# Optimization experiments

Hardware: AMD Instinct MI355X
Metric: run time of the kernel (lower is better)

## Reference

```python
import jax, jax.numpy as jnp
import numpy as np

MODES = 2
N = 6000
KNN = 15
NODES = 512
LC = 3  # number of hidden layers
SCALE = 0.05


def _gen_coo(n, knn):
    # One (row, col) pair per CK_inputs entry: node i couples to 2*(knn+1)
    # neighbors i-knn .. i+knn+1, clipped to valid range. Duplicates at the
    # boundaries are summed on scatter (matches torch sparse coalesce()).
    offsets = np.arange(-knn, knn + 2)            # 2*(knn+1) offsets
    rows = np.repeat(np.arange(n), 2 * (knn + 1))
    cols = np.clip((np.arange(n)[:, None] + offsets[None, :]).reshape(-1), 0, n - 1)
    return rows.astype(np.int32), cols.astype(np.int32)


def setup_inputs() -> dict:
    key = jax.random.key(0)
    k0, k1, k2, k3 = jax.random.split(key, 4)
    CK_inputs = jax.random.normal(k0, (N, 2 * (KNN + 1), 3), dtype=jnp.float32)
    W_in = (jax.random.normal(k1, (3, NODES), dtype=jnp.float32) * SCALE)
    b_in = jnp.zeros((NODES,), dtype=jnp.float32)
    Wh = (jax.random.normal(k2, (LC, NODES, NODES), dtype=jnp.float32) * SCALE)
    bh = jnp.zeros((LC, NODES), dtype=jnp.float32)
    W_out = (jax.random.normal(k3, (NODES, MODES ** 2), dtype=jnp.float32) * SCALE)
    b_out = jnp.zeros((MODES ** 2,), dtype=jnp.float32)
    rows_np, cols_np = _gen_coo(N, KNN)
    return {
        "CK_inputs": CK_inputs,
        "W_in": W_in, "b_in": b_in,
        "Wh": Wh, "bh": bh,
        "W_out": W_out, "b_out": b_out,
        "rows": jnp.asarray(rows_np), "cols": jnp.asarray(cols_np),
    }


def reference(CK_inputs, W_in, b_in, Wh, bh, W_out, b_out, rows, cols):
    n = CK_inputs.shape[0]
    modes = int(np.sqrt(b_out.shape[0]))
    # MLP over all E = N*2*(Knn+1) couplings: [E,3] -> [E, modes^2]
    x = CK_inputs.reshape(-1, 3)
    h = jax.nn.relu(x @ W_in + b_in)
    for l in range(Wh.shape[0]):  # small fixed layer count
        h = jax.nn.relu(h @ Wh[l] + bh[l])
    vals = (h @ W_out + b_out).reshape(-1, modes, modes)  # [E, mi, mj]
    # Fused scatter-add: original builds modes^2 sparse COO tensors with
    # indices (r*modes+mi, c*modes+mj), sums, coalesces, densifies. That is
    # exactly dense[r, mi, c, mj] += vals[e, mi, mj].
    dense = jnp.zeros((n, modes, n, modes), dtype=CK_inputs.dtype)
    dense = dense.at[rows, :, cols, :].add(vals)
    return dense.reshape(n * modes, n * modes)
```

## Files before the change

kernel.cpp:

```cpp
#include <hip/hip_runtime.h>

#define NN     6000
#define KNN    15
#define EPB    32
#define HID    512
#define NLAYER 3
#define OUTDIM 12000
#define MB     96
#define NTH    512
#define NKT    16
#define NG     (NLAYER * NKT)

typedef _Float16 half8  __attribute__((ext_vector_type(8)));
typedef _Float16 half4v __attribute__((ext_vector_type(4)));
typedef float    floatx4 __attribute__((ext_vector_type(4)));

__global__ void prep_weights(const float* __restrict__ Wh, _Float16* __restrict__ Wt)
{
    const int blk = blockIdx.x;
    const int ln  = threadIdx.x;
    const int nt  = blk & 31;
    const int kt  = (blk >> 5) & 15;
    const int l   = blk >> 9;
    const int lc  = ln & 15, lg = ln >> 4;
    const float* src = Wh + (size_t)l * HID * HID
                          + (size_t)(kt * 32 + lg * 8) * HID + nt * 16 + lc;
    half8 v;
#pragma unroll
    for (int j = 0; j < 8; ++j) v[j] = (_Float16)src[(size_t)j * HID];
    *(half8*)(Wt + (size_t)blk * 512 + ln * 8) = v;
}

__global__ __launch_bounds__(NTH, 1)
void mlp_mfma_kernel(const float* __restrict__ CK,
                     const float* __restrict__ W_in,
                     const float* __restrict__ b_in,
                     const float* __restrict__ bh,
                     const float* __restrict__ W_out,
                     const float* __restrict__ b_out,
                     const _Float16* __restrict__ Wt,
                     float4* __restrict__ vals)
{
    extern __shared__ float4 smem4[];
    _Float16* Ah = (_Float16*)smem4;
    __shared__ float xs[MB * 3];

    const int t  = threadIdx.x;
    const int w  = t >> 6;
    const int ln = t & 63;
    const int lc = ln & 15;
    const int lg = ln >> 4;
    const int kbase = lg * 8;
    const int swzA  = (lc & 7) << 3;

    const half8* __restrict__ Wt8 = (const half8*)Wt + (size_t)(w * 4) * 64 + ln;

    half8 bA[4], bB[4];
#pragma unroll
    for (int nf = 0; nf < 4; ++nf) bA[nf] = Wt8[(size_t)0 * 2048 + nf * 64];
#pragma unroll
    for (int nf = 0; nf < 4; ++nf) bB[nf] = Wt8[(size_t)1 * 2048 + nf * 64];

    if (t < MB * 3) xs[t] = CK[(size_t)blockIdx.x * (MB * 3) + t];
    __syncthreads();

    {
        const int j0 = t;
        const float wi0 = W_in[j0], wi1 = W_in[HID + j0], wi2 = W_in[2 * HID + j0];
        const float bi  = b_in[j0];
#pragma unroll 8
        for (int r = 0; r < MB; ++r) {
            float a = fmaf(xs[r * 3 + 2], wi2,
                      fmaf(xs[r * 3 + 1], wi1,
                      fmaf(xs[r * 3 + 0], wi0, bi)));
            Ah[r * HID + (j0 ^ ((r & 7) << 3))] = (_Float16)fmaxf(a, 0.f);
        }
    }
    __syncthreads();

#define KSTEP(G, RCUR) do {                                                    \
        half8 a_[6];                                                           \
        const int kb_ = ((G) & 15) * 32 + kbase;                               \
        _Pragma("unroll")                                                      \
        for (int mf_ = 0; mf_ < 6; ++mf_)                                      \
            a_[mf_] = *(const half8*)&Ah[(mf_ * 16 + lc) * HID + (kb_ ^ swzA)];\
        __builtin_amdgcn_s_setprio(1);                                         \
        _Pragma("unroll")                                                      \
        for (int mf_ = 0; mf_ < 6; ++mf_)                                      \
            _Pragma("unroll")                                                  \
            for (int nf_ = 0; nf_ < 4; ++nf_)                                  \
                acc[mf_][nf_] = __builtin_amdgcn_mfma_f32_16x16x32_f16(        \
                    RCUR[nf_], a_[mf_], acc[mf_][nf_], 0, 0, 0);               \
        __builtin_amdgcn_s_setprio(0);                                         \
        if ((G) + 2 < NG) {                                                    \
            _Pragma("unroll")                                                  \
            for (int nf_ = 0; nf_ < 4; ++nf_)                                  \
                RCUR[nf_] = Wt8[(size_t)((G) + 2) * 2048 + nf_ * 64];          \
        }                                                                      \
    } while (0)

    for (int layer = 0; layer < NLAYER; ++layer) {
        const float* __restrict__ bias = bh + layer * HID;

        floatx4 acc[6][4];
#pragma unroll
        for (int nf = 0; nf < 4; ++nf) {
            const floatx4 bv = *(const floatx4*)&bias[w * 64 + nf * 16 + lg * 4];
#pragma unroll
            for (int mf = 0; mf < 6; ++mf) acc[mf][nf] = bv;
        }

#pragma unroll
        for (int kt2 = 0; kt2 < NKT; kt2 += 2) {
            const int g = layer * NKT + kt2;
            KSTEP(g,     bA);
            KSTEP(g + 1, bB);
        }

        __syncthreads();
#pragma unroll
        for (int mf = 0; mf < 6; ++mf) {
            const int r = mf * 16 + lc;
#pragma unroll
            for (int nf = 0; nf < 4; ++nf) {
                const int n0 = w * 64 + nf * 16 + lg * 4;
                half4v h4;
#pragma unroll
                for (int j = 0; j < 4; ++j)
                    h4[j] = (_Float16)fmaxf(acc[mf][nf][j], 0.f);
                *(half4v*)&Ah[r * HID + (n0 ^ swzA)] = h4;
            }
        }
        __syncthreads();
    }

    {
        const int s = t & 7;
        const float4 bo = *(const float4*)b_out;
#pragma unroll
        for (int pass = 0; pass < 2; ++pass) {
            const int rr = pass * 64 + (t >> 3);
            if (rr < MB) {
                const int swzr = (rr & 7) << 3;
                float p0 = 0.f, p1 = 0.f, p2 = 0.f, p3 = 0.f;
                for (int i = 0; i < HID / 8; ++i) {
                    const int k = s + i * 8;
                    const float hv = (float)Ah[rr * HID + (k ^ swzr)];
                    const floatx4 wv = *(const floatx4*)&W_out[k * 4];
                    p0 = fmaf(hv, wv[0], p0);
                    p1 = fmaf(hv, wv[1], p1);
                    p2 = fmaf(hv, wv[2], p2);
                    p3 = fmaf(hv, wv[3], p3);
                }
#pragma unroll
                for (int m = 1; m < 8; m <<= 1) {
                    p0 += __shfl_xor(p0, m, 64);
                    p1 += __shfl_xor(p1, m, 64);
                    p2 += __shfl_xor(p2, m, 64);
                    p3 += __shfl_xor(p3, m, 64);
                }
                if (s == 0)
                    vals[(size_t)blockIdx.x * MB + rr] =
                        make_float4(p0 + bo.x, p1 + bo.y, p2 + bo.z, p3 + bo.w);
            }
        }
    }
}

__global__ __launch_bounds__(256, 8)
void write_out(const float4* __restrict__ vals, float* __restrict__ out)
{
    const int n = blockIdx.x;
    const int t = threadIdx.x;
    __shared__ float4 v[EPB];
    __shared__ float  band[2][2 * EPB];

    if (t < EPB) v[t] = vals[(size_t)n * EPB + t];
    const int cmin  = (n - KNN < 0) ? 0 : n - KNN;
    const int cmax  = (n + KNN + 1 > NN - 1) ? NN - 1 : n + KNN + 1;
    const int width = cmax - cmin + 1;
    __syncthreads();

    if (t < width) {
        const int c = cmin + t;
        int e_lo, e_hi;
        if (c == 0)           { e_lo = 0;                  e_hi = KNN - n; }
        else if (c == NN - 1) { e_lo = (NN - 1) - n + KNN; e_hi = EPB - 1; }
        else                  { e_lo = e_hi = c - n + KNN; }
        float s0 = 0.f, s1 = 0.f, s2 = 0.f, s3 = 0.f;
        for (int e = e_lo; e <= e_hi; ++e) {
            const float4 pv = v[e];
            s0 += pv.x; s1 += pv.y; s2 += pv.z; s3 += pv.w;
        }
        band[0][2 * t] = s0; band[0][2 * t + 1] = s1;
        band[1][2 * t] = s2; band[1][2 * t + 1] = s3;
    }
    __syncthreads();

    const int j0 = 2 * cmin;
    const int w2 = 2 * width;
#pragma unroll
    for (int mi = 0; mi < 2; ++mi) {
        float* rowp = out + (size_t)(2 * n + mi) * OUTDIM;
        for (int q = t; q < OUTDIM / 4; q += 256) {
            const int j = 4 * q;
            floatx4 o;
            o[0] = ((unsigned)(j + 0 - j0) < (unsigned)w2) ? band[mi][j + 0 - j0] : 0.f;
            o[1] = ((unsigned)(j + 1 - j0) < (unsigned)w2) ? band[mi][j + 1 - j0] : 0.f;
            o[2] = ((unsigned)(j + 2 - j0) < (unsigned)w2) ? band[mi][j + 2 - j0] : 0.f;
            o[3] = ((unsigned)(j + 3 - j0) < (unsigned)w2) ? band[mi][j + 3 - j0] : 0.f;
            __builtin_nontemporal_store(o, (floatx4*)(rowp + j));
        }
    }
}

extern "C" void kernel_launch(void* const* d_in, const int* in_sizes, int n_in,
                              void* d_out, int out_size, void* d_ws, size_t ws_size,
                              hipStream_t stream) {
    const float* CK    = (const float*)d_in[0];
    const float* W_in  = (const float*)d_in[1];
    const float* b_in  = (const float*)d_in[2];
    const float* Wh    = (const float*)d_in[3];
    const float* bh    = (const float*)d_in[4];
    const float* W_out = (const float*)d_in[5];
    const float* b_out = (const float*)d_in[6];
    float* out = (float*)d_out;

    _Float16* Wt   = (_Float16*)d_ws;
    float4*   vals = (float4*)((char*)d_ws + (size_t)3 * HID * HID * sizeof(_Float16));

    (void)ws_size;
    hipFuncSetAttribute((const void*)mlp_mfma_kernel,
                        hipFuncAttributeMaxDynamicSharedMemorySize, 98304);

    prep_weights<<<NLAYER * 16 * 32, 64, 0, stream>>>(Wh, Wt);
    mlp_mfma_kernel<<<NN / 3, NTH, 98304, stream>>>(CK, W_in, b_in, bh, W_out, b_out, Wt, vals);
    write_out<<<NN, 256, 0, stream>>>(vals, out);
}
```

Measured before the change: 412.8 us.

## Store activations in MFMA fragment-ordered LDS layout instead of XOR swizzle

Activations in LDS are reorganized so each (k-tile, m-fragment) block of 16 rows x 32 k values is stored contiguously in the order each lane reads it for the MFMA A operand. The input layer, the inter-layer writeback and the output projection are all rewritten to produce and consume this layout. This turns A-fragment loads into linear 16-byte-per-lane reads without XOR address math and lets the output layer read half8 vectors. The input layer now computes 8 contiguous k values per lane, with more W_in global loads per thread, and the writeback stores may see different bank patterns.

Measured after the change: 535.6 us. +29.7%, slower.

```diff
diff --git a/kernel.cpp b/kernel.cpp
--- a/kernel.cpp
+++ b/kernel.cpp
@@ -50,8 +50,6 @@
     const int ln = t & 63;
     const int lc = ln & 15;
     const int lg = ln >> 4;
-    const int kbase = lg * 8;
-    const int swzA  = (lc & 7) << 3;
 
     const half8* __restrict__ Wt8 = (const half8*)Wt + (size_t)(w * 4) * 64 + ln;
 
@@ -65,25 +63,32 @@
     __syncthreads();
 
     {
-        const int j0 = t;
-        const float wi0 = W_in[j0], wi1 = W_in[HID + j0], wi2 = W_in[2 * HID + j0];
-        const float bi  = b_in[j0];
-#pragma unroll 8
-        for (int r = 0; r < MB; ++r) {
-            float a = fmaf(xs[r * 3 + 2], wi2,
-                      fmaf(xs[r * 3 + 1], wi1,
-                      fmaf(xs[r * 3 + 0], wi0, bi)));
-            Ah[r * HID + (j0 ^ ((r & 7) << 3))] = (_Float16)fmaxf(a, 0.f);
+#pragma unroll
+        for (int i = 0; i < 12; ++i) {
+            const int b  = w + i * 8;
+            const int kt = b / 6, mf = b - kt * 6;
+            const int r  = mf * 16 + lc;
+            const int k0 = kt * 32 + lg * 8;
+            const float x0 = xs[r * 3 + 0], x1 = xs[r * 3 + 1], x2 = xs[r * 3 + 2];
+            half8 h;
+#pragma unroll
+            for (int j = 0; j < 8; ++j) {
+                const int k = k0 + j;
+                float a = fmaf(x2, W_in[2 * HID + k],
+                          fmaf(x1, W_in[HID + k],
+                          fmaf(x0, W_in[k], b_in[k])));
+                h[j] = (_Float16)fmaxf(a, 0.f);
+            }
+            *(half8*)&Ah[b * 512 + ln * 8] = h;
         }
     }
     __syncthreads();
 
 #define KSTEP(G, RCUR) do {                                                    \
         half8 a_[6];                                                           \
-        const int kb_ = ((G) & 15) * 32 + kbase;                               \
         _Pragma("unroll")                                                      \
         for (int mf_ = 0; mf_ < 6; ++mf_)                                      \
-            a_[mf_] = *(const half8*)&Ah[(mf_ * 16 + lc) * HID + (kb_ ^ swzA)];\
+            a_[mf_] = *(const half8*)&Ah[((((G) & 15) * 6 + mf_) << 9) + ln * 8]; \
         __builtin_amdgcn_s_setprio(1);                                         \
         _Pragma("unroll")                                                      \
         for (int mf_ = 0; mf_ < 6; ++mf_)                                      \
@@ -120,15 +125,15 @@
         __syncthreads();
 #pragma unroll
         for (int mf = 0; mf < 6; ++mf) {
-            const int r = mf * 16 + lc;
 #pragma unroll
             for (int nf = 0; nf < 4; ++nf) {
-                const int n0 = w * 64 + nf * 16 + lg * 4;
                 half4v h4;
 #pragma unroll
                 for (int j = 0; j < 4; ++j)
                     h4[j] = (_Float16)fmaxf(acc[mf][nf][j], 0.f);
-                *(half4v*)&Ah[r * HID + (n0 ^ swzA)] = h4;
+                const int ktp  = w * 2 + (nf >> 1);
+                const int slot = lc + 16 * (2 * (nf & 1) + (lg >> 1));
+                *(half4v*)&Ah[((ktp * 6 + mf) << 9) + slot * 8 + (lg & 1) * 4] = h4;
             }
         }
         __syncthreads();
@@ -141,16 +146,23 @@
         for (int pass = 0; pass < 2; ++pass) {
             const int rr = pass * 64 + (t >> 3);
             if (rr < MB) {
-                const int swzr = (rr & 7) << 3;
+                const int mf = rr >> 4, rl = rr & 15;
                 float p0 = 0.f, p1 = 0.f, p2 = 0.f, p3 = 0.f;
-                for (int i = 0; i < HID / 8; ++i) {
-                    const int k = s + i * 8;
-                    const float hv = (float)Ah[rr * HID + (k ^ swzr)];
-                    const floatx4 wv = *(const floatx4*)&W_out[k * 4];
-                    p0 = fmaf(hv, wv[0], p0);
-                    p1 = fmaf(hv, wv[1], p1);
-                    p2 = fmaf(hv, wv[2], p2);
-                    p3 = fmaf(hv, wv[3], p3);
+#pragma unroll
+                for (int i = 0; i < 8; ++i) {
+                    const int kb2 = i * 8 + s;
+                    const half8 hv8 = *(const half8*)
+                        &Ah[(((kb2 >> 2) * 6 + mf) << 9) + (rl + 16 * (kb2 & 3)) * 8];
+                    const int k0 = kb2 * 8;
+#pragma unroll
+                    for (int p = 0; p < 8; ++p) {
+                        const float hv = (float)hv8[p];
+                        const floatx4 wv = *(const floatx4*)&W_out[(k0 + p) * 4];
+                        p0 = fmaf(hv, wv[0], p0);
+                        p1 = fmaf(hv, wv[1], p1);
+                        p2 = fmaf(hv, wv[2], p2);
+                        p3 = fmaf(hv, wv[3], p3);
+                    }
                 }
 #pragma unroll
                 for (int m = 1; m < 8; m <<= 1) {
```

## Fuse dense scatter output into MLP kernel, overlapping zero stores with MFMA layers

Applied to the files above, without the earlier changes.

Removes the separate write_out kernel and the intermediate vals buffer. Each MLP block now writes the zero background of its six output rows with nontemporal stores interleaved between its hidden-layer MFMA loops, so the large output write overlaps compute. After the MLP it reduces edge values into band sums in shared memory and writes only the band window with scalar stores. The trade-offs are extra shared memory and extra store instructions inside the compute-bound loop, and the band writes are scalar rather than vectorized.

Result: faster. 383.6 us (-7.1%).

```diff
diff --git a/kernel.cpp b/kernel.cpp
--- a/kernel.cpp
+++ b/kernel.cpp
@@ -39,11 +39,13 @@
                      const float* __restrict__ W_out,
                      const float* __restrict__ b_out,
                      const _Float16* __restrict__ Wt,
-                     float4* __restrict__ vals)
+                     float* __restrict__ out)
 {
     extern __shared__ float4 smem4[];
     _Float16* Ah = (_Float16*)smem4;
-    __shared__ float xs[MB * 3];
+    __shared__ float  xs[MB * 3];
+    __shared__ float4 edgeval[MB];
+    __shared__ float  bandv[3][2][80];
 
     const int t  = threadIdx.x;
     const int w  = t >> 6;
@@ -52,6 +54,23 @@
     const int lg = ln >> 4;
     const int kbase = lg * 8;
     const int swzA  = (lc & 7) << 3;
+    const int m  = blockIdx.x;
+
+    const floatx4 z4 = (floatx4){0.f, 0.f, 0.f, 0.f};
+#define ZROW(Q) do {                                                           \
+        const int n_   = 3 * m + ((Q) >> 1);                                   \
+        const int cmin_ = (n_ - KNN < 0) ? 0 : n_ - KNN;                       \
+        const int cmax_ = (n_ + KNN + 1 > NN - 1) ? NN - 1 : n_ + KNN + 1;     \
+        const int end_  = 2 * cmin_ + 2 * (cmax_ - cmin_ + 1);                 \
+        const int wlo_  = (2 * cmin_) & ~3;                                    \
+        const int whi_  = (end_ + 3) & ~3;                                     \
+        float* rowp_ = out + (size_t)(6 * m + (Q)) * OUTDIM;                   \
+        for (int i_ = t; i_ < OUTDIM / 4; i_ += NTH) {                         \
+            const int j_ = 4 * i_;                                             \
+            if (j_ < wlo_ || j_ >= whi_)                                       \
+                __builtin_nontemporal_store(z4, (floatx4*)(rowp_ + j_));       \
+        }                                                                      \
+    } while (0)
 
     const half8* __restrict__ Wt8 = (const half8*)Wt + (size_t)(w * 4) * 64 + ln;
 
@@ -61,7 +80,7 @@
 #pragma unroll
     for (int nf = 0; nf < 4; ++nf) bB[nf] = Wt8[(size_t)1 * 2048 + nf * 64];
 
-    if (t < MB * 3) xs[t] = CK[(size_t)blockIdx.x * (MB * 3) + t];
+    if (t < MB * 3) xs[t] = CK[(size_t)m * (MB * 3) + t];
     __syncthreads();
 
     {
@@ -110,6 +129,9 @@
             for (int mf = 0; mf < 6; ++mf) acc[mf][nf] = bv;
         }
 
+        ZROW(layer * 2);
+        ZROW(layer * 2 + 1);
+
 #pragma unroll
         for (int kt2 = 0; kt2 < NKT; kt2 += 2) {
             const int g = layer * NKT + kt2;
@@ -153,63 +175,58 @@
                     p3 = fmaf(hv, wv[3], p3);
                 }
 #pragma unroll
-                for (int m = 1; m < 8; m <<= 1) {
-                    p0 += __shfl_xor(p0, m, 64);
-                    p1 += __shfl_xor(p1, m, 64);
-                    p2 += __shfl_xor(p2, m, 64);
-                    p3 += __shfl_xor(p3, m, 64);
+                for (int mm = 1; mm < 8; mm <<= 1) {
+                    p0 += __shfl_xor(p0, mm, 64);
+                    p1 += __shfl_xor(p1, mm, 64);
+                    p2 += __shfl_xor(p2, mm, 64);
+                    p3 += __shfl_xor(p3, mm, 64);
                 }
                 if (s == 0)
-                    vals[(size_t)blockIdx.x * MB + rr] =
-                        make_float4(p0 + bo.x, p1 + bo.y, p2 + bo.z, p3 + bo.w);
+                    edgeval[rr] = make_float4(p0 + bo.x, p1 + bo.y,
+                                              p2 + bo.z, p3 + bo.w);
             }
         }
     }
-}
-
-__global__ __launch_bounds__(256, 8)
-void write_out(const float4* __restrict__ vals, float* __restrict__ out)
-{
-    const int n = blockIdx.x;
-    const int t = threadIdx.x;
-    __shared__ float4 v[EPB];
-    __shared__ float  band[2][2 * EPB];
-
-    if (t < EPB) v[t] = vals[(size_t)n * EPB + t];
-    const int cmin  = (n - KNN < 0) ? 0 : n - KNN;
-    const int cmax  = (n + KNN + 1 > NN - 1) ? NN - 1 : n + KNN + 1;
-    const int width = cmax - cmin + 1;
-    __syncthreads();
-
-    if (t < width) {
-        const int c = cmin + t;
-        int e_lo, e_hi;
-        if (c == 0)           { e_lo = 0;                  e_hi = KNN - n; }
-        else if (c == NN - 1) { e_lo = (NN - 1) - n + KNN; e_hi = EPB - 1; }
-        else                  { e_lo = e_hi = c - n + KNN; }
-        float s0 = 0.f, s1 = 0.f, s2 = 0.f, s3 = 0.f;
-        for (int e = e_lo; e <= e_hi; ++e) {
-            const float4 pv = v[e];
-            s0 += pv.x; s1 += pv.y; s2 += pv.z; s3 += pv.w;
-        }
-        band[0][2 * t] = s0; band[0][2 * t + 1] = s1;
-        band[1][2 * t] = s2; band[1][2 * t + 1] = s3;
-    }
-    __syncthreads();
-
-    const int j0 = 2 * cmin;
-    const int w2 = 2 * width;
-#pragma unroll
-    for (int mi = 0; mi < 2; ++mi) {
-        float* rowp = out + (size_t)(2 * n + mi) * OUTDIM;
-        for (int q = t; q < OUTDIM / 4; q += 256) {
-            const int j = 4 * q;
-            floatx4 o;
-            o[0] = ((unsigned)(j + 0 - j0) < (unsigned)w2) ? band[mi][j + 0 - j0] : 0.f;
-            o[1] = ((unsigned)(j + 1 - j0) < (unsigned)w2) ? band[mi][j + 1 - j0] : 0.f;
-            o[2] = ((unsigned)(j + 2 - j0) < (unsigned)w2) ? band[mi][j + 2 - j0] : 0.f;
-            o[3] = ((unsigned)(j + 3 - j0) < (unsigned)w2) ? band[mi][j + 3 - j0] : 0.f;
-            __builtin_nontemporal_store(o, (floatx4*)(rowp + j));
+    __syncthreads();
+
+    if (t < 96) {
+        const int nd = t >> 5, ci = t & 31;
+        const int n  = 3 * m + nd;
+        const int cmin  = (n - KNN < 0) ? 0 : n - KNN;
+        const int cmax  = (n + KNN + 1 > NN - 1) ? NN - 1 : n + KNN + 1;
+        const int width = cmax - cmin + 1;
+        if (ci < width) {
+            const int c = cmin + ci;
+            int e_lo, e_hi;
+            if (c == 0)           { e_lo = 0;                  e_hi = KNN - n; }
+            else if (c == NN - 1) { e_lo = (NN - 1) - n + KNN; e_hi = EPB - 1; }
+            else                  { e_lo = e_hi = c - n + KNN; }
+            float s0 = 0.f, s1 = 0.f, s2 = 0.f, s3 = 0.f;
+            for (int e = e_lo; e <= e_hi; ++e) {
+                const float4 pv = edgeval[nd * EPB + e];
+                s0 += pv.x; s1 += pv.y; s2 += pv.z; s3 += pv.w;
+            }
+            bandv[nd][0][2 * ci] = s0; bandv[nd][0][2 * ci + 1] = s1;
+            bandv[nd][1][2 * ci] = s2; bandv[nd][1][2 * ci + 1] = s3;
+        }
+    }
+    __syncthreads();
+
+    if (t < 6 * 80) {
+        const int q  = t / 80;
+        const int jl = t % 80;
+        const int nd = q >> 1, mi = q & 1;
+        const int n  = 3 * m + nd;
+        const int cmin  = (n - KNN < 0) ? 0 : n - KNN;
+        const int cmax  = (n + KNN + 1 > NN - 1) ? NN - 1 : n + KNN + 1;
+        const int end   = 2 * cmin + 2 * (cmax - cmin + 1);
+        const int wlo   = (2 * cmin) & ~3;
+        const int whi   = (end + 3) & ~3;
+        const int j     = wlo + jl;
+        if (j < whi) {
+            const bool inside = (j >= 2 * cmin) && (j < end);
+            const float v = inside ? bandv[nd][mi][j - 2 * cmin] : 0.f;
+            out[(size_t)(6 * m + q) * OUTDIM + j] = v;
         }
     }
 }
@@ -226,14 +243,13 @@
     const float* b_out = (const float*)d_in[6];
     float* out = (float*)d_out;
 
-    _Float16* Wt   = (_Float16*)d_ws;
-    float4*   vals = (float4*)((char*)d_ws + (size_t)3 * HID * HID * sizeof(_Float16));
+    _Float16* Wt = (_Float16*)d_ws;
 
     (void)ws_size;
     hipFuncSetAttribute((const void*)mlp_mfma_kernel,
                         hipFuncAttributeMaxDynamicSharedMemorySize, 98304);
 
     prep_weights<<<NLAYER * 16 * 32, 64, 0, stream>>>(Wh, Wt);
-    mlp_mfma_kernel<<<NN / 3, NTH, 98304, stream>>>(CK, W_in, b_in, bh, W_out, b_out, Wt, vals);
-    write_out<<<NN, 256, 0, stream>>>(vals, out);
+    mlp_mfma_kernel<<<NN / 3, NTH, 98304, stream>>>(CK, W_in, b_in, bh,
+                                                    W_out, b_out, Wt, out);
 }
```
